# Performance work log

Measured on AMD Instinct MI355X. Metric: run time of the kernel, lower is better.

The kernel has to match this reference:

```python
import jax, jax.numpy as jnp
import numpy as np

NUM_POINTS = 200_000
AMBIENT_DIM = 3
NUM_THETAS = 128
RESOLUTION = 128
BATCH_SIZE = 64


def setup_inputs() -> dict:
    key = jax.random.key(0)
    kx, kv, kb = jax.random.split(key, 3)
    x = jax.random.normal(kx, (NUM_POINTS, AMBIENT_DIM), dtype=jnp.float32)
    # unit-norm direction vectors, columns of v [ambient_dim, num_thetas]
    v = jax.random.normal(kv, (AMBIENT_DIM, NUM_THETAS), dtype=jnp.float32)
    v = v / jnp.linalg.norm(v, axis=0, keepdims=True)
    batch = jnp.sort(jax.random.randint(kb, (NUM_POINTS,), 0, BATCH_SIZE, dtype=jnp.int32))
    return {"x": x, "v": v, "batch": batch, "resolution": RESOLUTION, "batch_size": BATCH_SIZE}


def reference(x, v, batch, resolution, batch_size):
    # projected heights: [N, T]
    nh = x @ v
    N, T = nh.shape
    # bin heights over the unit ball [-1, 1] into `resolution` bins (fast ECT bincount)
    bins = jnp.clip(jnp.floor((nh + 1.0) * (0.5 * resolution)).astype(jnp.int32), 0, resolution - 1)
    theta = jnp.arange(T, dtype=jnp.int32)  # [T]
    # flat scatter index over (batch, bin, theta)
    flat = (batch.astype(jnp.int32)[:, None] * resolution + bins) * T + theta[None, :]
    hist = jnp.zeros((batch_size * resolution * T,), dtype=x.dtype)
    hist = hist.at[flat.reshape(-1)].add(1.0)
    hist = hist.reshape(batch_size, resolution, T)
    # cumulative histogram along the filtration (resolution) axis = ECT
    ect = jnp.cumsum(hist, axis=1)  # [B, resolution, num_thetas]
    return ect
```

## Files before the change

### kernel.cpp

```cpp
#include <hip/hip_runtime.h>


constexpr int N_PTS    = 200000;
constexpr int T        = 128;
constexpr int R        = 128;
constexpr int B        = 64;
constexpr int SPLIT_T  = 8;
constexpr int TT       = T / SPLIT_T;
constexpr int NTHREADS = 1024;
constexpr int TG       = 4;
constexpr int PL       = NTHREADS / TG;

__global__ __launch_bounds__(NTHREADS, 8)
void FastEctLayer_73065983639654_kernel(const float* __restrict__ x,
                                        const float* __restrict__ v,
                                        const int*   __restrict__ batch,
                                        float*       __restrict__ out) {
    __shared__ unsigned int hist[R * 32];
    __shared__ unsigned int partial[64 * TT];
    __shared__ unsigned int sum8[8 * TT];
    __shared__ int s_range[2];

    const int tid    = threadIdx.x;
    const int tg     = tid & (TG - 1);
    const int pl     = tid >> 2;
    const int bat    = blockIdx.x / SPLIT_T;
    const int theta0 = (blockIdx.x % SPLIT_T) * TT;
    const int sub16  = ((pl >> 2) & 1) << 4;

    for (int i = tid; i < R * 32; i += NTHREADS) hist[i] = 0u;

    const int wave = tid >> 6, lane = tid & 63;
    if (wave < 2) {
        const int val = bat + wave;
        int lo = 0, hi = N_PTS;
        while (lo < hi) {
            const int step = (hi - lo + 63) >> 6;
            const int pos  = lo + lane * step;
            const bool pred = (pos < hi) && (batch[pos] < val);
            const unsigned long long m = __ballot(pred);
            const int k = __popcll(m);
            if (k == 0) {
                hi = lo;
            } else {
                const int nlo = lo + (k - 1) * step + 1;
                hi = min(hi, lo + k * step);
                lo = nlo;
            }
        }
        if (lane == 0) s_range[wave] = lo;
    }

    int   offj[4];
    float vv0[4], vv1[4], vv2[4];
#pragma unroll
    for (int j = 0; j < 4; ++j) {
        const int tl = (4 * tg + j + pl) & (TT - 1);
        offj[j] = sub16 + tl;
        vv0[j] = v[0 * T + theta0 + tl] * 64.0f;
        vv1[j] = v[1 * T + theta0 + tl] * 64.0f;
        vv2[j] = v[2 * T + theta0 + tl] * 64.0f;
    }

    __syncthreads();
    const int start = s_range[0];
    const int end   = s_range[1];

    const int a0      = start & ~3;
    const int nchunks = (end - a0 + 3) >> 2;
    const float4* __restrict__ X4 = (const float4*)x;
    const int cbase = (a0 >> 2) * 3;

    auto process4 = [&](int pbase, float4 f0, float4 f1, float4 f2) {
        const float px[4] = {f0.x, f0.w, f1.z, f2.y};
        const float py[4] = {f0.y, f1.x, f1.w, f2.z};
        const float pz[4] = {f0.z, f1.y, f2.x, f2.w};
        if (pbase >= start && pbase + 3 < end) {
#pragma unroll
            for (int i = 0; i < 4; ++i) {
#pragma unroll
                for (int j = 0; j < 4; ++j) {
                    const float bf = fmaf(px[i], vv0[j], fmaf(py[i], vv1[j],
                                     fmaf(pz[i], vv2[j], 64.0f)));
                    int bin = (int)bf;
                    bin = min(max(bin, 0), R - 1);
                    atomicAdd(&hist[(bin << 5) + offj[j]], 1u);
                }
            }
        } else {
#pragma unroll
            for (int i = 0; i < 4; ++i) {
                const int p = pbase + i;
                if (p >= start && p < end) {
#pragma unroll
                    for (int j = 0; j < 4; ++j) {
                        const float bf = fmaf(px[i], vv0[j], fmaf(py[i], vv1[j],
                                         fmaf(pz[i], vv2[j], 64.0f)));
                        int bin = (int)bf;
                        bin = min(max(bin, 0), R - 1);
                        atomicAdd(&hist[(bin << 5) + offj[j]], 1u);
                    }
                }
            }
        }
    };

    for (int c = pl; c < nchunks; c += PL) {
        const float4 f0 = X4[cbase + 3 * c];
        const float4 f1 = X4[cbase + 3 * c + 1];
        const float4 f2 = X4[cbase + 3 * c + 2];
        process4(a0 + 4 * c, f0, f1, f2);
    }

    __syncthreads();

    const int tl  = tid & (TT - 1);
    const int seg = tid >> 4;
    const int r0  = seg * 2;
    unsigned int csum = 0;
#pragma unroll
    for (int r = r0; r < r0 + 2; ++r)
        csum += hist[(r << 5) + tl] + hist[(r << 5) + 16 + tl];
    partial[seg * TT + tl] = csum;
    __syncthreads();

    if (tid < 8 * TT) {
        const int g = tid >> 4;
        unsigned int s = 0;
#pragma unroll
        for (int k = 0; k < 8; ++k) s += partial[(g * 8 + k) * TT + tl];
        sum8[g * TT + tl] = s;
    }
    __syncthreads();

    unsigned int run = 0;
    const int g = seg >> 3;
    for (int gg = 0; gg < g; ++gg)        run += sum8[gg * TT + tl];
    for (int s2 = g * 8; s2 < seg; ++s2)  run += partial[s2 * TT + tl];
#pragma unroll
    for (int r = r0; r < r0 + 2; ++r) {
        run += hist[(r << 5) + tl] + hist[(r << 5) + 16 + tl];
        out[((size_t)bat * R + r) * T + theta0 + tl] = (float)run;
    }
}

extern "C" void kernel_launch(void* const* d_in, const int* in_sizes, int n_in,
                              void* d_out, int out_size, void* d_ws, size_t ws_size,
                              hipStream_t stream) {
    const float* x     = (const float*)d_in[0];
    const float* v     = (const float*)d_in[1];
    const int*   batch = (const int*)d_in[2];
    float*       out   = (float*)d_out;

    dim3 grid(B * SPLIT_T);
    dim3 block(NTHREADS);
    hipLaunchKernelGGL(FastEctLayer_73065983639654_kernel, grid, block, 0, stream,
                       x, v, batch, out);
}
```

Measured before the change: 72.32 us.

## Halve theta split, drop duplicated histogram copies, add two-deep prefetch of points

Each block now covers 32 thetas instead of 16, so the grid is halved and every batch segment is read from global memory half as often. The histogram no longer keeps two copies per theta: all threads share one R×32 array, which raises atomic contention per shared-memory word. The point loop now prefetches two chunks ahead to hide global load latency. The launch-bounds occupancy hint is removed and the scan stages are resized to match the new layout.

```diff
diff --git a/kernel.cpp b/kernel.cpp
--- a/kernel.cpp
+++ b/kernel.cpp
@@ -5,32 +5,29 @@
 constexpr int T        = 128;
 constexpr int R        = 128;
 constexpr int B        = 64;
-constexpr int SPLIT_T  = 8;
+constexpr int SPLIT_T  = 4;
 constexpr int TT       = T / SPLIT_T;
 constexpr int NTHREADS = 1024;
-constexpr int TG       = 4;
+constexpr int TG       = 8;
 constexpr int PL       = NTHREADS / TG;
+constexpr int SUBS     = NTHREADS / TT;
+constexpr int RCH      = R / SUBS;
 
-__global__ __launch_bounds__(NTHREADS, 8)
+__global__ __launch_bounds__(NTHREADS)
 void FastEctLayer_73065983639654_kernel(const float* __restrict__ x,
                                         const float* __restrict__ v,
                                         const int*   __restrict__ batch,
                                         float*       __restrict__ out) {
-    __shared__ unsigned int hist[R * 32];
-    __shared__ unsigned int partial[64 * TT];
-    __shared__ unsigned int sum8[8 * TT];
+    __shared__ unsigned int hist[R * TT];
+    __shared__ unsigned int partial[SUBS * TT];
+    __shared__ unsigned int grp[4 * TT];
     __shared__ int s_range[2];
 
-    const int tid    = threadIdx.x;
-    const int tg     = tid & (TG - 1);
-    const int pl     = tid >> 2;
-    const int bat    = blockIdx.x / SPLIT_T;
-    const int theta0 = (blockIdx.x % SPLIT_T) * TT;
-    const int sub16  = ((pl >> 2) & 1) << 4;
+    const int tid  = threadIdx.x;
+    const int wave = tid >> 6, lane = tid & 63;
+    const int bat    = blockIdx.x >> 2;
+    const int theta0 = (blockIdx.x & 3) * TT;
 
-    for (int i = tid; i < R * 32; i += NTHREADS) hist[i] = 0u;
-
-    const int wave = tid >> 6, lane = tid & 63;
     if (wave < 2) {
         const int val = bat + wave;
         int lo = 0, hi = N_PTS;
@@ -51,12 +48,16 @@
         if (lane == 0) s_range[wave] = lo;
     }
 
-    int   offj[4];
+    for (int i = tid; i < R * TT; i += NTHREADS) hist[i] = 0u;
+
+    const int tg = tid & (TG - 1);
+    const int pl = tid >> 3;
+    int   tlj[4];
     float vv0[4], vv1[4], vv2[4];
 #pragma unroll
     for (int j = 0; j < 4; ++j) {
         const int tl = (4 * tg + j + pl) & (TT - 1);
-        offj[j] = sub16 + tl;
+        tlj[j] = tl;
         vv0[j] = v[0 * T + theta0 + tl] * 64.0f;
         vv1[j] = v[1 * T + theta0 + tl] * 64.0f;
         vv2[j] = v[2 * T + theta0 + tl] * 64.0f;
@@ -84,7 +85,7 @@
                                      fmaf(pz[i], vv2[j], 64.0f)));
                     int bin = (int)bf;
                     bin = min(max(bin, 0), R - 1);
-                    atomicAdd(&hist[(bin << 5) + offj[j]], 1u);
+                    atomicAdd(&hist[(bin << 5) + tlj[j]], 1u);
                 }
             }
         } else {
@@ -98,48 +99,57 @@
                                          fmaf(pz[i], vv2[j], 64.0f)));
                         int bin = (int)bf;
                         bin = min(max(bin, 0), R - 1);
-                        atomicAdd(&hist[(bin << 5) + offj[j]], 1u);
+                        atomicAdd(&hist[(bin << 5) + tlj[j]], 1u);
                     }
                 }
             }
         }
     };
 
-    for (int c = pl; c < nchunks; c += PL) {
-        const float4 f0 = X4[cbase + 3 * c];
-        const float4 f1 = X4[cbase + 3 * c + 1];
-        const float4 f2 = X4[cbase + 3 * c + 2];
-        process4(a0 + 4 * c, f0, f1, f2);
+    int c = pl;
+    float4 A0, A1, A2, B0, B1, B2;
+    bool haveA = (c < nchunks);
+    if (haveA) { A0 = X4[cbase + 3*c]; A1 = X4[cbase + 3*c + 1]; A2 = X4[cbase + 3*c + 2]; }
+    bool haveB = (c + PL < nchunks);
+    if (haveB) { B0 = X4[cbase + 3*(c+PL)]; B1 = X4[cbase + 3*(c+PL) + 1]; B2 = X4[cbase + 3*(c+PL) + 2]; }
+    while (haveA) {
+        const int cn = c + 2 * PL;
+        const bool haveC = (cn < nchunks);
+        float4 C0, C1, C2;
+        if (haveC) { C0 = X4[cbase + 3*cn]; C1 = X4[cbase + 3*cn + 1]; C2 = X4[cbase + 3*cn + 2]; }
+        process4(a0 + 4 * c, A0, A1, A2);
+        A0 = B0; A1 = B1; A2 = B2; haveA = haveB;
+        B0 = C0; B1 = C1; B2 = C2; haveB = haveC;
+        c += PL;
     }
 
     __syncthreads();
 
     const int tl  = tid & (TT - 1);
-    const int seg = tid >> 4;
-    const int r0  = seg * 2;
+    const int seg = tid >> 5;
+    const int r0  = seg * RCH;
     unsigned int csum = 0;
 #pragma unroll
-    for (int r = r0; r < r0 + 2; ++r)
-        csum += hist[(r << 5) + tl] + hist[(r << 5) + 16 + tl];
+    for (int r = r0; r < r0 + RCH; ++r) csum += hist[(r << 5) + tl];
     partial[seg * TT + tl] = csum;
     __syncthreads();
 
-    if (tid < 8 * TT) {
-        const int g = tid >> 4;
+    if (tid < 4 * TT) {
+        const int g = tid >> 5;
         unsigned int s = 0;
 #pragma unroll
         for (int k = 0; k < 8; ++k) s += partial[(g * 8 + k) * TT + tl];
-        sum8[g * TT + tl] = s;
+        grp[g * TT + tl] = s;
     }
     __syncthreads();
 
     unsigned int run = 0;
     const int g = seg >> 3;
-    for (int gg = 0; gg < g; ++gg)        run += sum8[gg * TT + tl];
+    for (int gg = 0; gg < g; ++gg)        run += grp[gg * TT + tl];
     for (int s2 = g * 8; s2 < seg; ++s2)  run += partial[s2 * TT + tl];
 #pragma unroll
-    for (int r = r0; r < r0 + 2; ++r) {
-        run += hist[(r << 5) + tl] + hist[(r << 5) + 16 + tl];
+    for (int r = r0; r < r0 + RCH; ++r) {
+        run += hist[(r << 5) + tl];
         out[((size_t)bat * R + r) * T + theta0 + tl] = (float)run;
     }
 }
```

Measured after the change: 70.73 us. -2.2%, faster.
